# Performance work log

Measured on AMD Instinct MI355X. Metric: run time of the kernel, lower is better.

## Reference

```python
import jax, jax.numpy as jnp
import numpy as np

B, S, RNN, ATTH = 256, 196, 1024, 512  # batch, att_size, rnn_size, att_h_size


def setup_inputs() -> dict:
    key = jax.random.key(0)
    k1, k2, k3, k4, k5, k6, k7 = jax.random.split(key, 7)
    h = jax.random.normal(k1, (B, RNN), dtype=jnp.float32)
    att_feats = jax.random.normal(k2, (B, S, RNN), dtype=jnp.float32)
    p_att_feats = jax.random.normal(k3, (B, S, ATTH), dtype=jnp.float32)
    # learned params (torch nn.Linear: y = x @ W.T + b)
    w_h2att = jax.random.normal(k4, (ATTH, RNN), dtype=jnp.float32) / np.sqrt(RNN)
    b_h2att = jax.random.normal(k5, (ATTH,), dtype=jnp.float32) * 0.01
    w_alpha = jax.random.normal(k6, (1, ATTH), dtype=jnp.float32) / np.sqrt(ATTH)
    b_alpha = jax.random.normal(k7, (1,), dtype=jnp.float32) * 0.01
    return {
        "h": h,
        "att_feats": att_feats,
        "p_att_feats": p_att_feats,
        "w_h2att": w_h2att,
        "b_h2att": b_h2att,
        "w_alpha": w_alpha,
        "b_alpha": b_alpha,
    }


def reference(h, att_feats, p_att_feats, w_h2att, b_h2att, w_alpha, b_alpha):
    # att_h = h2att(h): [B, ATTH]
    att_h = h @ w_h2att.T + b_h2att
    # additive combine + tanh: [B, S, ATTH]
    dot = jnp.tanh(p_att_feats + att_h[:, None, :])
    # alpha_net: [B, S]
    scores = jnp.einsum("bsa,a->bs", dot, w_alpha[0]) + b_alpha[0]
    weight = jax.nn.softmax(scores, axis=1)
    # weighted sum of att_feats: [B, RNN]
    att_res = jnp.einsum("bs,bsd->bd", weight, att_feats)
    return att_res
```

## Files before the change

### kernel.cpp

```cpp
#include <hip/hip_runtime.h>
#include <cstddef>

static constexpr int kB    = 256;
static constexpr int kS    = 196;
static constexpr int kRNN  = 1024;
static constexpr int kATTH = 512;
static constexpr int kQ    = 4;
static constexpr int kSC   = kS / kQ;

static constexpr size_t kOffAttH  = 0;
static constexpr size_t kOffEsc   = kOffAttH + (size_t)kB * kATTH;
static constexpr size_t kOffPart  = kOffEsc + (size_t)kB * kS;

__device__ __forceinline__ float fast_tanh(float x) {
    x = fminf(12.0f, fmaxf(-12.0f, x));
    float e = __expf(2.0f * x);
    return __fdividef(e - 1.0f, e + 1.0f);
}

__device__ __forceinline__ float dot8t(const float4 p0, const float4 p1,
                                       const float4 ah0, const float4 ah1,
                                       const float4 wa0, const float4 wa1) {
    float r;
    r  = fast_tanh(p0.x + ah0.x) * wa0.x;
    r += fast_tanh(p0.y + ah0.y) * wa0.y;
    r += fast_tanh(p0.z + ah0.z) * wa0.z;
    r += fast_tanh(p0.w + ah0.w) * wa0.w;
    r += fast_tanh(p1.x + ah1.x) * wa1.x;
    r += fast_tanh(p1.y + ah1.y) * wa1.y;
    r += fast_tanh(p1.z + ah1.z) * wa1.z;
    r += fast_tanh(p1.w + ah1.w) * wa1.w;
    return r;
}

__global__ __launch_bounds__(1024) void k1_atth(
    const float* __restrict__ h, const float* __restrict__ w_h2att,
    const float* __restrict__ b_h2att, float* __restrict__ att_h) {
    const int b = blockIdx.x;
    const int tid = threadIdx.x;
    const int lane = tid & 63;
    const int wave = tid >> 6;

    const float* hb = &h[(size_t)b * kRNN];
    const int k0 = lane << 2;
    const float4 h0 = *(const float4*)&hb[k0];
    const float4 h1 = *(const float4*)&hb[k0 + 256];
    const float4 h2 = *(const float4*)&hb[k0 + 512];
    const float4 h3 = *(const float4*)&hb[k0 + 768];
    const int abase = wave << 5;
#pragma unroll 2
    for (int r = 0; r < 32; ++r) {
        const int a = abase + r;
        const float* wr = &w_h2att[(size_t)a * kRNN + k0];
        const float4 x0 = *(const float4*)(wr);
        const float4 x1 = *(const float4*)(wr + 256);
        const float4 x2 = *(const float4*)(wr + 512);
        const float4 x3 = *(const float4*)(wr + 768);
        float d;
        d  = x0.x * h0.x + x0.y * h0.y + x0.z * h0.z + x0.w * h0.w;
        d += x1.x * h1.x + x1.y * h1.y + x1.z * h1.z + x1.w * h1.w;
        d += x2.x * h2.x + x2.y * h2.y + x2.z * h2.z + x2.w * h2.w;
        d += x3.x * h3.x + x3.y * h3.y + x3.z * h3.z + x3.w * h3.w;
#pragma unroll
        for (int off = 32; off > 0; off >>= 1) d += __shfl_xor(d, off, 64);
        if (lane == 0) att_h[(size_t)b * kATTH + a] = d + b_h2att[a];
    }
}

__global__ __launch_bounds__(256) void k2_scores(
    const float* __restrict__ p_att, const float* __restrict__ att_h,
    const float* __restrict__ w_alpha, const float* __restrict__ b_alpha,
    float* __restrict__ escore) {
    const int b = blockIdx.x >> 2;
    const int q = blockIdx.x & 3;
    const int tid = threadIdx.x;
    const int lane = tid & 63;
    const int wave = tid >> 6;

    const int col = lane << 3;
    const float4 ah0 = *(const float4*)&att_h[(size_t)b * kATTH + col];
    const float4 ah1 = *(const float4*)&att_h[(size_t)b * kATTH + col + 4];
    const float4 wa0 = *(const float4*)&w_alpha[col];
    const float4 wa1 = *(const float4*)&w_alpha[col + 4];
    const float balpha = b_alpha[0];

    float sw = fabsf(wa0.x) + fabsf(wa0.y) + fabsf(wa0.z) + fabsf(wa0.w) +
               fabsf(wa1.x) + fabsf(wa1.y) + fabsf(wa1.z) + fabsf(wa1.w);
#pragma unroll
    for (int off = 32; off > 0; off >>= 1) sw += __shfl_xor(sw, off, 64);
    const float ebias = balpha - (sw + fabsf(balpha));

    const float* pbase = &p_att[(size_t)b * kS * kATTH + col];
    const int send = q * kSC + kSC;
    int s = q * kSC + wave;
    float4 p0, p1;
    {
        const float* p = pbase + (size_t)s * kATTH;
        p0 = *(const float4*)p;
        p1 = *(const float4*)(p + 4);
    }
    while (true) {
        const int sn = s + 4;
        const bool more = sn < send;
        float4 np0, np1;
        if (more) {
            const float* p = pbase + (size_t)sn * kATTH;
            np0 = *(const float4*)p;
            np1 = *(const float4*)(p + 4);
        }
        float r = dot8t(p0, p1, ah0, ah1, wa0, wa1);
#pragma unroll
        for (int off = 32; off > 0; off >>= 1) r += __shfl_xor(r, off, 64);
        if (lane == 0) escore[(size_t)b * kS + s] = __expf(r + ebias);
        if (!more) break;
        s = sn;
        p0 = np0; p1 = np1;
    }
}

__global__ __launch_bounds__(256) void k3_pv(
    const float* __restrict__ att_feats, const float* __restrict__ escore,
    float* __restrict__ part) {
    const int b = blockIdx.x >> 2;
    const int q = blockIdx.x & 3;
    const int tid = threadIdx.x;

    __shared__ float sW[kSC];
    if (tid < kSC) sW[tid] = escore[(size_t)b * kS + q * kSC + tid];
    __syncthreads();

    const float* af =
        &att_feats[((size_t)b * kS + q * kSC) * kRNN + (tid << 2)];
    float4 acc = {0.f, 0.f, 0.f, 0.f};
#pragma unroll 7
    for (int i = 0; i < kSC; ++i) {
        const float w = sW[i];
        const float4 v = *(const float4*)(af + (size_t)i * kRNN);
        acc.x += w * v.x; acc.y += w * v.y;
        acc.z += w * v.z; acc.w += w * v.w;
    }
    *(float4*)&part[((size_t)(b * kQ + q)) * kRNN + (tid << 2)] = acc;
}

__global__ __launch_bounds__(256) void k4_combine(
    const float* __restrict__ part, const float* __restrict__ escore,
    float* __restrict__ out) {
    const int b = blockIdx.x;
    const int tid = threadIdx.x;
    const int lane = tid & 63;
    const int wave = tid >> 6;

    __shared__ float sPart[4];
    float v = (tid < kS) ? escore[(size_t)b * kS + tid] : 0.f;
#pragma unroll
    for (int off = 32; off > 0; off >>= 1) v += __shfl_xor(v, off, 64);
    if (lane == 0) sPart[wave] = v;
    __syncthreads();
    const float inv = __fdividef(1.0f, sPart[0] + sPart[1] + sPart[2] + sPart[3]);

    const float* pb = &part[(size_t)b * kQ * kRNN + (tid << 2)];
    const float4 a0 = *(const float4*)(pb);
    const float4 a1 = *(const float4*)(pb + kRNN);
    const float4 a2 = *(const float4*)(pb + 2 * kRNN);
    const float4 a3 = *(const float4*)(pb + 3 * kRNN);
    float4 o;
    o.x = (a0.x + a1.x + a2.x + a3.x) * inv;
    o.y = (a0.y + a1.y + a2.y + a3.y) * inv;
    o.z = (a0.z + a1.z + a2.z + a3.z) * inv;
    o.w = (a0.w + a1.w + a2.w + a3.w) * inv;
    *(float4*)&out[(size_t)b * kRNN + (tid << 2)] = o;
}

extern "C" void kernel_launch(void* const* d_in, const int* in_sizes, int n_in,
                              void* d_out, int out_size, void* d_ws, size_t ws_size,
                              hipStream_t stream) {
    const float* h         = (const float*)d_in[0];
    const float* att_feats = (const float*)d_in[1];
    const float* p_att     = (const float*)d_in[2];
    const float* w_h2att   = (const float*)d_in[3];
    const float* b_h2att   = (const float*)d_in[4];
    const float* w_alpha   = (const float*)d_in[5];
    const float* b_alpha   = (const float*)d_in[6];
    float* out = (float*)d_out;

    float* ws     = (float*)d_ws;
    float* att_h  = ws + kOffAttH;
    float* escore = ws + kOffEsc;
    float* part   = ws + kOffPart;

    k1_atth<<<kB, 1024, 0, stream>>>(h, w_h2att, b_h2att, att_h);
    k2_scores<<<kB * kQ, 256, 0, stream>>>(p_att, att_h, w_alpha, b_alpha, escore);
    k3_pv<<<kB * kQ, 256, 0, stream>>>(att_feats, escore, part);
    k4_combine<<<kB, 256, 0, stream>>>(part, escore, out);
}
```

Baseline: 398.3 us.

## Fuse score and weighted-sum kernels, split att_h GEMV into smaller blocks

Merges the score kernel and the weighted-sum kernel into one. Exponentiated scores stay in shared memory and each block writes only a per-quarter partial sum, so the combine kernel no longer re-reduces all scores. The att_h kernel is split into four 256-thread blocks per batch row, and the att_feats loop batches seven loads before the FMAs to raise memory-level parallelism. The cost is that the tail of each score loop re-reads a clamped row, and h gets reloaded by four blocks.

```diff
diff --git a/kernel.cpp b/kernel.cpp
--- a/kernel.cpp
+++ b/kernel.cpp
@@ -8,9 +8,9 @@
 static constexpr int kQ    = 4;
 static constexpr int kSC   = kS / kQ;
 
-static constexpr size_t kOffAttH  = 0;
-static constexpr size_t kOffEsc   = kOffAttH + (size_t)kB * kATTH;
-static constexpr size_t kOffPart  = kOffEsc + (size_t)kB * kS;
+static constexpr size_t kOffAttH = 0;
+static constexpr size_t kOffEsum = kOffAttH + (size_t)kB * kATTH;
+static constexpr size_t kOffPart = kOffEsum + (size_t)kB * kQ;
 
 __device__ __forceinline__ float fast_tanh(float x) {
     x = fminf(12.0f, fmaxf(-12.0f, x));
@@ -33,10 +33,11 @@
     return r;
 }
 
-__global__ __launch_bounds__(1024) void k1_atth(
+__global__ __launch_bounds__(256, 4) void k1_atth(
     const float* __restrict__ h, const float* __restrict__ w_h2att,
     const float* __restrict__ b_h2att, float* __restrict__ att_h) {
-    const int b = blockIdx.x;
+    const int b  = blockIdx.x >> 2;
+    const int rq = blockIdx.x & 3;
     const int tid = threadIdx.x;
     const int lane = tid & 63;
     const int wave = tid >> 6;
@@ -47,7 +48,7 @@
     const float4 h1 = *(const float4*)&hb[k0 + 256];
     const float4 h2 = *(const float4*)&hb[k0 + 512];
     const float4 h3 = *(const float4*)&hb[k0 + 768];
-    const int abase = wave << 5;
+    const int abase = rq * 128 + wave * 32;
 #pragma unroll 2
     for (int r = 0; r < 32; ++r) {
         const int a = abase + r;
@@ -67,15 +68,19 @@
     }
 }
 
-__global__ __launch_bounds__(256) void k2_scores(
-    const float* __restrict__ p_att, const float* __restrict__ att_h,
-    const float* __restrict__ w_alpha, const float* __restrict__ b_alpha,
-    float* __restrict__ escore) {
+__global__ __launch_bounds__(256, 4) void k23_score_pv(
+    const float* __restrict__ att_feats, const float* __restrict__ p_att,
+    const float* __restrict__ att_h, const float* __restrict__ w_alpha,
+    const float* __restrict__ b_alpha, float* __restrict__ esum,
+    float* __restrict__ part) {
     const int b = blockIdx.x >> 2;
     const int q = blockIdx.x & 3;
     const int tid = threadIdx.x;
     const int lane = tid & 63;
     const int wave = tid >> 6;
+
+    __shared__ float sE[kSC];
+    __shared__ float sEw[4];
 
     const int col = lane << 3;
     const float4 ah0 = *(const float4*)&att_h[(size_t)b * kATTH + col];
@@ -90,73 +95,58 @@
     for (int off = 32; off > 0; off >>= 1) sw += __shfl_xor(sw, off, 64);
     const float ebias = balpha - (sw + fabsf(balpha));
 
-    const float* pbase = &p_att[(size_t)b * kS * kATTH + col];
-    const int send = q * kSC + kSC;
-    int s = q * kSC + wave;
-    float4 p0, p1;
-    {
-        const float* p = pbase + (size_t)s * kATTH;
-        p0 = *(const float4*)p;
-        p1 = *(const float4*)(p + 4);
-    }
-    while (true) {
-        const int sn = s + 4;
-        const bool more = sn < send;
-        float4 np0, np1;
-        if (more) {
-            const float* p = pbase + (size_t)sn * kATTH;
-            np0 = *(const float4*)p;
-            np1 = *(const float4*)(p + 4);
-        }
+    const float* pbase = &p_att[((size_t)b * kS + (size_t)q * kSC) * kATTH + col];
+    int s = wave;
+    float4 p0 = *(const float4*)(pbase + (size_t)s * kATTH);
+    float4 p1 = *(const float4*)(pbase + (size_t)s * kATTH + 4);
+    const int nIter = (wave == 0) ? 13 : 12;
+    float esumw = 0.f;
+    for (int i = 0; i < nIter; ++i) {
+        int sn = s + 4;
+        sn = (sn > kSC - 1) ? (kSC - 1) : sn;
+        const float4 np0 = *(const float4*)(pbase + (size_t)sn * kATTH);
+        const float4 np1 = *(const float4*)(pbase + (size_t)sn * kATTH + 4);
         float r = dot8t(p0, p1, ah0, ah1, wa0, wa1);
 #pragma unroll
         for (int off = 32; off > 0; off >>= 1) r += __shfl_xor(r, off, 64);
-        if (lane == 0) escore[(size_t)b * kS + s] = __expf(r + ebias);
-        if (!more) break;
+        if (lane == 0) {
+            const float e = __expf(r + ebias);
+            sE[s] = e;
+            esumw += e;
+        }
         s = sn;
         p0 = np0; p1 = np1;
     }
-}
-
-__global__ __launch_bounds__(256) void k3_pv(
-    const float* __restrict__ att_feats, const float* __restrict__ escore,
-    float* __restrict__ part) {
-    const int b = blockIdx.x >> 2;
-    const int q = blockIdx.x & 3;
-    const int tid = threadIdx.x;
-
-    __shared__ float sW[kSC];
-    if (tid < kSC) sW[tid] = escore[(size_t)b * kS + q * kSC + tid];
+    if (lane == 0) sEw[wave] = esumw;
     __syncthreads();
+    if (tid == 0) esum[b * kQ + q] = sEw[0] + sEw[1] + sEw[2] + sEw[3];
 
     const float* af =
-        &att_feats[((size_t)b * kS + q * kSC) * kRNN + (tid << 2)];
+        &att_feats[((size_t)b * kS + (size_t)q * kSC) * kRNN + (tid << 2)];
     float4 acc = {0.f, 0.f, 0.f, 0.f};
-#pragma unroll 7
-    for (int i = 0; i < kSC; ++i) {
-        const float w = sW[i];
-        const float4 v = *(const float4*)(af + (size_t)i * kRNN);
-        acc.x += w * v.x; acc.y += w * v.y;
-        acc.z += w * v.z; acc.w += w * v.w;
+    for (int o = 0; o < 7; ++o) {
+        float4 v[7];
+#pragma unroll
+        for (int j = 0; j < 7; ++j)
+            v[j] = *(const float4*)(af + (size_t)(o * 7 + j) * kRNN);
+#pragma unroll
+        for (int j = 0; j < 7; ++j) {
+            const float w = sE[o * 7 + j];
+            acc.x += w * v[j].x; acc.y += w * v[j].y;
+            acc.z += w * v[j].z; acc.w += w * v[j].w;
+        }
     }
     *(float4*)&part[((size_t)(b * kQ + q)) * kRNN + (tid << 2)] = acc;
 }
 
 __global__ __launch_bounds__(256) void k4_combine(
-    const float* __restrict__ part, const float* __restrict__ escore,
+    const float* __restrict__ part, const float* __restrict__ esum,
     float* __restrict__ out) {
     const int b = blockIdx.x;
     const int tid = threadIdx.x;
-    const int lane = tid & 63;
-    const int wave = tid >> 6;
 
-    __shared__ float sPart[4];
-    float v = (tid < kS) ? escore[(size_t)b * kS + tid] : 0.f;
-#pragma unroll
-    for (int off = 32; off > 0; off >>= 1) v += __shfl_xor(v, off, 64);
-    if (lane == 0) sPart[wave] = v;
-    __syncthreads();
-    const float inv = __fdividef(1.0f, sPart[0] + sPart[1] + sPart[2] + sPart[3]);
+    const float* es = &esum[b * kQ];
+    const float inv = __fdividef(1.0f, es[0] + es[1] + es[2] + es[3]);
 
     const float* pb = &part[(size_t)b * kQ * kRNN + (tid << 2)];
     const float4 a0 = *(const float4*)(pb);
@@ -183,13 +173,13 @@
     const float* b_alpha   = (const float*)d_in[6];
     float* out = (float*)d_out;
 
-    float* ws     = (float*)d_ws;
-    float* att_h  = ws + kOffAttH;
-    float* escore = ws + kOffEsc;
-    float* part   = ws + kOffPart;
+    float* ws    = (float*)d_ws;
+    float* att_h = ws + kOffAttH;
+    float* esum  = ws + kOffEsum;
+    float* part  = ws + kOffPart;
 
-    k1_atth<<<kB, 1024, 0, stream>>>(h, w_h2att, b_h2att, att_h);
-    k2_scores<<<kB * kQ, 256, 0, stream>>>(p_att, att_h, w_alpha, b_alpha, escore);
-    k3_pv<<<kB * kQ, 256, 0, stream>>>(att_feats, escore, part);
-    k4_combine<<<kB, 256, 0, stream>>>(part, escore, out);
+    k1_atth<<<kB * 4, 256, 0, stream>>>(h, w_h2att, b_h2att, att_h);
+    k23_score_pv<<<kB * kQ, 256, 0, stream>>>(att_feats, p_att, att_h, w_alpha,
+                                              b_alpha, esum, part);
+    k4_combine<<<kB, 256, 0, stream>>>(part, esum, out);
 }
```

Measured after the change: 387.5 us. 1.03x faster.
